# Optimization experiments

Measured on AMD Instinct MI355X. Metric: run time of the kernel, lower is better.

The kernel has to match this reference:

```python
import jax, jax.numpy as jnp
import numpy as np

LAYERS, BLOCKS = 10, 3
NL = LAYERS * BLOCKS
DC, RC, SC, CLASSES, K = 128, 128, 256, 256, 2
SR = 4096  # number of output samples sliced from the end
N, L, EN = 4, 8192, 16


def _conv1x1(x, w):
    # x: [N, Cin, L], w: [Cout, Cin] -> [N, Cout, L]
    return jnp.einsum('ncl,oc->nol', x, w)


def _condition(x, enc):
    # x: [N, C, L], enc: [N, C, En], L % En == 0; tiled periodic add (faithful to the view trick)
    n, c, l = x.shape
    en = enc.shape[2]
    return (x.reshape(n, c, l // en, en) + enc[:, :, None, :]).reshape(n, c, l)


def _dilated_causal_conv(x, w, d):
    # kernel_size=2 causal dilated conv. x: [N, Cin, L], w: [Cout, Cin, 2]
    xs = jnp.pad(x, ((0, 0), (0, 0), (d, 0)))[:, :, :x.shape[2]]  # x delayed by d
    return jnp.einsum('ncl,oc->nol', xs, w[:, :, 0]) + jnp.einsum('ncl,oc->nol', x, w[:, :, 1])


def setup_inputs() -> dict:
    key = jax.random.key(0)
    ks = jax.random.split(key, 12)
    s = 0.05
    return {
        'x': jax.random.normal(ks[0], (N, CLASSES, L), jnp.float32),
        'en': jax.random.normal(ks[1], (N, CLASSES, EN), jnp.float32),
        'start1_w': jax.random.normal(ks[2], (RC, CLASSES), jnp.float32) * s,
        'start2_w': jax.random.normal(ks[3], (SC, RC), jnp.float32) * s,
        'cond_w': jax.random.normal(ks[4], (NL, 2 * DC, CLASSES), jnp.float32) * s,
        'dil_w': jax.random.normal(ks[5], (NL, 2 * DC, RC, K), jnp.float32) * s,
        'res_w': jax.random.normal(ks[6], (NL, RC, DC), jnp.float32) * s,
        'skip_w': jax.random.normal(ks[7], (NL, SC, DC), jnp.float32) * s,
        'end1_w': jax.random.normal(ks[8], (CLASSES, SC), jnp.float32) * s,
        'end1_b': jnp.zeros((CLASSES,), jnp.float32),
        'end2_w': jax.random.normal(ks[9], (CLASSES, CLASSES), jnp.float32) * s,
        'end2_b': jnp.zeros((CLASSES,), jnp.float32),
    }


def reference(x, en, start1_w, start2_w, cond_w, dil_w, res_w, skip_w,
              end1_w, end1_b, end2_w, end2_b):
    l = _conv1x1(x, start1_w)          # [N, RC, L]
    s = _conv1x1(l, start2_w)          # [N, SC, L]
    for i in range(NL):
        dil = 2 ** (i % LAYERS)
        d = _dilated_causal_conv(l, dil_w[i], dil)      # [N, 2*DC, L]
        d = _condition(d, _conv1x1(en, cond_w[i]))
        g = jax.nn.sigmoid(d[:, :DC]) * jnp.tanh(d[:, DC:])  # gated, [N, DC, L]
        l = l + _conv1x1(g, res_w[i])
        s = s + _conv1x1(g, skip_w[i])
    s = jax.nn.relu(s)
    s = _conv1x1(s, end1_w) + end1_b[None, :, None]
    s = _condition(s, _conv1x1(en, end2_w) + end2_b[None, :, None])
    s = jax.nn.relu(s)
    return s[:, :, -SR:]
```

## Files before the change

kernel.cpp:

```cpp
#include <hip/hip_runtime.h>

typedef __bf16 bf16_t;
typedef __bf16 bf16x8 __attribute__((ext_vector_type(8)));
typedef __bf16 bf16x4 __attribute__((ext_vector_type(4)));
typedef float  f32x4  __attribute__((ext_vector_type(4)));
typedef int    i32x4  __attribute__((ext_vector_type(4)));

#define PL 136
#define PX 264

__device__ __forceinline__ f32x4 mfma16(bf16x8 a, bf16x8 b, f32x4 c) {
    return __builtin_amdgcn_mfma_f32_16x16x32_bf16(a, b, c, 0, 0, 0);
}

__device__ __forceinline__ void conv8(const float* __restrict__ src,
                                      bf16_t* __restrict__ dst,
                                      int g, int M, int K) {
    int MK8 = (M * K) >> 3;
    int lay = g / MK8;
    int r = g - lay * MK8;
    int lane = r & 63, rest = r >> 6;
    int KB = K >> 5;
    int kb = rest % KB, mt = rest / KB;
    int m = mt * 16 + (lane & 15);
    int k = kb * 32 + ((lane >> 4) << 3);
    const float* s = src + (size_t)lay * M * K + (size_t)m * K + k;
    f32x4 v0 = *(const f32x4*)s;
    f32x4 v1 = *(const f32x4*)(s + 4);
    bf16x8 o;
    o[0] = (bf16_t)v0[0]; o[1] = (bf16_t)v0[1]; o[2] = (bf16_t)v0[2]; o[3] = (bf16_t)v0[3];
    o[4] = (bf16_t)v1[0]; o[5] = (bf16_t)v1[1]; o[6] = (bf16_t)v1[2]; o[7] = (bf16_t)v1[3];
    *(bf16x8*)(dst + (size_t)g * 8) = o;
}

__global__ __launch_bounds__(256) void k_prep(
                       const float* __restrict__ rw, const float* __restrict__ kw,
                       const float* __restrict__ s1w, const float* __restrict__ s2w,
                       const float* __restrict__ e1w, const float* __restrict__ dwt,
                       const float* __restrict__ cond_w, const float* __restrict__ end2_w,
                       const float* __restrict__ end2_b, const float* __restrict__ en,
                       bf16_t* __restrict__ Ares, bf16_t* __restrict__ Askp,
                       bf16_t* __restrict__ A1, bf16_t* __restrict__ A2,
                       bf16_t* __restrict__ Ae, bf16_t* __restrict__ Adil,
                       float* __restrict__ cond_all, float* __restrict__ cond2) {
    if (blockIdx.x >= 1744) {
        __shared__ f32x4 en_s[1024];
        __shared__ f32x4 red[1024];
        int bi = blockIdx.x - 1744;
        int i = bi >> 4;
        int n = (bi >> 2) & 3;
        int og = bi & 3;
        int tid = threadIdx.x;
        const f32x4* ep = (const f32x4*)(en + (size_t)n * 4096);
        for (int idx = tid; idx < 1024; idx += 256) en_s[idx] = ep[idx];
        __syncthreads();
        int o_loc = tid >> 2, part = tid & 3;
        int o = og * 64 + o_loc;
        const float* W = (i < 30) ? cond_w + ((size_t)i * 256 + o) * 256
                                  : end2_w + (size_t)o * 256;
        const float* Wp = W + part * 64;
        f32x4 a0 = {0.f,0.f,0.f,0.f}, a1 = a0, a2 = a0, a3 = a0;
        for (int c = 0; c < 64; c += 4) {
            f32x4 wv = *(const f32x4*)(Wp + c);
            int cg = part * 64 + c;
            #pragma unroll
            for (int cc = 0; cc < 4; ++cc) {
                float wf = wv[cc];
                a0 += wf * en_s[(cg + cc) * 4 + 0];
                a1 += wf * en_s[(cg + cc) * 4 + 1];
                a2 += wf * en_s[(cg + cc) * 4 + 2];
                a3 += wf * en_s[(cg + cc) * 4 + 3];
            }
        }
        red[tid * 4 + 0] = a0; red[tid * 4 + 1] = a1;
        red[tid * 4 + 2] = a2; red[tid * 4 + 3] = a3;
        __syncthreads();
        if (tid < 64) {
            int o2 = og * 64 + tid;
            float bias = (i < 30) ? 0.f : end2_b[o2];
            float* dst = (i < 30) ? cond_all + (((size_t)i * 4 + n) * 256 + o2) * 16
                                  : cond2 + ((size_t)n * 256 + o2) * 16;
            f32x4* d4 = (f32x4*)dst;
            #pragma unroll
            for (int t = 0; t < 4; ++t) {
                f32x4 s = red[(tid * 4 + 0) * 4 + t] + red[(tid * 4 + 1) * 4 + t]
                        + red[(tid * 4 + 2) * 4 + t] + red[(tid * 4 + 3) * 4 + t];
                d4[t] = s + bias;
            }
        }
        return;
    }
    int g = blockIdx.x * 256 + threadIdx.x;
    if (g < 61440) { conv8(rw, Ares, g, 128, 128); return; }
    g -= 61440;
    if (g < 122880) { conv8(kw, Askp, g, 256, 128); return; }
    g -= 122880;
    if (g < 4096) { conv8(s1w, A1, g, 128, 256); return; }
    g -= 4096;
    if (g < 4096) { conv8(s2w, A2, g, 256, 128); return; }
    g -= 4096;
    if (g < 8192) { conv8(e1w, Ae, g, 256, 256); return; }
    g -= 8192;
    {
        int lay = g >> 13, r = g & 8191;
        int lane = r & 63, rest = r >> 6;
        int kb = rest & 7, mt = rest >> 3;
        int m = mt * 16 + (lane & 15);
        int k0 = kb * 32 + ((lane >> 4) << 3);
        int sel = (k0 < 128) ? 0 : 1;
        int kk = (k0 < 128) ? k0 : k0 - 128;
        const float* s = dwt + (((size_t)lay * 256 + m) * 128 + kk) * 2;
        f32x4 c0 = *(const f32x4*)(s);
        f32x4 c1 = *(const f32x4*)(s + 4);
        f32x4 c2 = *(const f32x4*)(s + 8);
        f32x4 c3 = *(const f32x4*)(s + 12);
        bf16x8 o;
        o[0] = (bf16_t)c0[sel];     o[1] = (bf16_t)c0[2 + sel];
        o[2] = (bf16_t)c1[sel];     o[3] = (bf16_t)c1[2 + sel];
        o[4] = (bf16_t)c2[sel];     o[5] = (bf16_t)c2[2 + sel];
        o[6] = (bf16_t)c3[sel];     o[7] = (bf16_t)c3[2 + sel];
        *(bf16x8*)(Adil + (size_t)lay * 65536 + (size_t)r * 8) = o;
    }
}

__global__ __launch_bounds__(512, 4) void k_start(
    const float* __restrict__ x, bf16_t* __restrict__ la, float* __restrict__ sbuf,
    const bf16_t* __restrict__ A1, const bf16_t* __restrict__ A2, int t_base)
{
    __shared__ __align__(16) bf16_t xt[64 * PX];
    __shared__ __align__(16) bf16_t l0[64 * PL];
    int tid = threadIdx.x;
    int n = blockIdx.y, t0 = t_base + blockIdx.x * 64;
    int lane = tid & 63, w = tid >> 6, i16 = lane & 15, q = lane >> 4;
    f32x4 z = {0.f,0.f,0.f,0.f};
    {
        int t = tid & 63;
        for (int c = tid >> 6; c < 256; c += 8)
            xt[t * PX + c] = (bf16_t)x[((size_t)n * 256 + c) * 8192 + t0 + t];
    }
    __syncthreads();
    f32x4 acc[4] = {z,z,z,z};
    #pragma unroll
    for (int kb = 0; kb < 8; ++kb) {
        int koff = kb * 32 + q * 8;
        bf16x8 bf[4];
        #pragma unroll
        for (int nt = 0; nt < 4; ++nt)
            bf[nt] = *(const bf16x8*)(xt + (nt * 16 + i16) * PX + koff);
        bf16x8 af = *(const bf16x8*)(A1 + (((size_t)w * 8 + kb) * 64 + lane) * 8);
        #pragma unroll
        for (int nt = 0; nt < 4; ++nt) acc[nt] = mfma16(af, bf[nt], acc[nt]);
    }
    #pragma unroll
    for (int nt = 0; nt < 4; ++nt)
        #pragma unroll
        for (int j = 0; j < 4; ++j)
            l0[(nt * 16 + i16) * PL + w * 16 + q * 4 + j] = (bf16_t)acc[nt][j];
    __syncthreads();
    {
        int r = tid >> 4, col = (tid & 15) * 8;
        #pragma unroll
        for (int p = 0; p < 2; ++p) {
            int rr = r + p * 32;
            *(i32x4*)(la + ((size_t)n * 8192 + t0 + rr) * 128 + col) =
                *(const i32x4*)(l0 + rr * PL + col);
        }
    }
    if (t0 >= 4096) {
        f32x4 a2[2][4] = {{z,z,z,z},{z,z,z,z}};
        #pragma unroll
        for (int kb = 0; kb < 4; ++kb) {
            int koff = kb * 32 + q * 8;
            bf16x8 bf[4];
            #pragma unroll
            for (int nt = 0; nt < 4; ++nt)
                bf[nt] = *(const bf16x8*)(l0 + (nt * 16 + i16) * PL + koff);
            #pragma unroll
            for (int mt2 = 0; mt2 < 2; ++mt2) {
                bf16x8 af = *(const bf16x8*)(A2 + ((((size_t)2 * w + mt2) * 4 + kb) * 64 + lane) * 8);
                #pragma unroll
                for (int nt = 0; nt < 4; ++nt) a2[mt2][nt] = mfma16(af, bf[nt], a2[mt2][nt]);
            }
        }
        float* sp = sbuf + (size_t)n * 256 * 4096 + (t0 - 4096);
        #pragma unroll
        for (int mt2 = 0; mt2 < 2; ++mt2)
            #pragma unroll
            for (int nt = 0; nt < 4; ++nt)
                #pragma unroll
                for (int j = 0; j < 4; ++j) {
                    int o = (2 * w + mt2) * 16 + q * 4 + j;
                    sp[(size_t)o * 4096 + nt * 16 + i16] = a2[mt2][nt][j];
                }
    }
}

template<int USEG>
__global__ __launch_bounds__(512, 4) void k_layer(
    const bf16_t* __restrict__ l_in, bf16_t* __restrict__ l_out,
    float* __restrict__ sbuf, bf16_t* __restrict__ Gl,
    const bf16_t* __restrict__ Ad, const bf16_t* __restrict__ Ar,
    const bf16_t* __restrict__ Ak, const float* __restrict__ condL,
    int dil, int t_base, int do_res)
{
    __shared__ __align__(16) bf16_t smA[64 * PL];
    __shared__ __align__(16) bf16_t sm2[32 * PL];
    int tid = threadIdx.x;
    int n = blockIdx.y, t0 = t_base + blockIdx.x * 32;
    int lane = tid & 63, w = tid >> 6, i16 = lane & 15, q = lane >> 4;
    f32x4 z = {0.f,0.f,0.f,0.f};
    const float* cond = condL + (size_t)n * 4096;
    int r = tid >> 4, col = (tid & 15) * 8;
    int c_base = w * 16 + q * 4;
    size_t base = (size_t)n * 8192;

    float cv_s[4], cv_t[4];
    #pragma unroll
    for (int j = 0; j < 4; ++j) {
        cv_s[j] = cond[(c_base + j) * 16 + i16];
        cv_t[j] = cond[(c_base + j + 128) * 16 + i16];
    }
    const bf16x8* AdF = (const bf16x8*)Ad;
    bf16x8 a_s[8], a_t[8];
    #pragma unroll
    for (int kb = 0; kb < 8; ++kb) {
        a_s[kb] = AdF[((size_t)w * 8 + kb) * 64 + lane];
        a_t[kb] = AdF[((size_t)(w + 8) * 8 + kb) * 64 + lane];
    }

    const bf16_t* curp;
    const bf16_t* delp;
    if (dil < 32) {
        int cnt = (32 + dil) * 16;
        for (int idx = tid; idx < cnt; idx += 512) {
            int rr = idx >> 4, c2 = (idx & 15) * 8;
            *(i32x4*)(smA + rr * PL + c2) =
                *(const i32x4*)(l_in + (base + t0 - dil + rr) * 128 + c2);
        }
        delp = smA; curp = smA + dil * PL;
    } else {
        *(i32x4*)(smA + r * PL + col) =
            *(const i32x4*)(l_in + (base + t0 + r) * 128 + col);
        int gp = t0 - dil + r;
        i32x4 v = {0, 0, 0, 0};
        if (gp >= 0) v = *(const i32x4*)(l_in + (base + gp) * 128 + col);
        *(i32x4*)(smA + (32 + r) * PL + col) = v;
        curp = smA; delp = smA + 32 * PL;
    }
    __syncthreads();

    f32x4 accs[2] = {z,z}, acct[2] = {z,z};
    #pragma unroll
    for (int kb = 0; kb < 8; ++kb) {
        const bf16_t* bsrc = (kb < 4) ? delp : curp;
        int koff = (kb & 3) * 32 + q * 8;
        bf16x8 bf[2];
        #pragma unroll
        for (int nt = 0; nt < 2; ++nt)
            bf[nt] = *(const bf16x8*)(bsrc + (nt * 16 + i16) * PL + koff);
        #pragma unroll
        for (int nt = 0; nt < 2; ++nt) {
            accs[nt] = mfma16(a_s[kb], bf[nt], accs[nt]);
            acct[nt] = mfma16(a_t[kb], bf[nt], acct[nt]);
        }
    }

    const bf16x8* ArF = (const bf16x8*)Ar;
    bf16x8 ar[4];
    if (do_res) {
        #pragma unroll
        for (int kb = 0; kb < 4; ++kb)
            ar[kb] = ArF[((size_t)w * 4 + kb) * 64 + lane];
    }

    {
        #pragma unroll
        for (int nt = 0; nt < 2; ++nt) {
            bf16x4 g4;
            #pragma unroll
            for (int j = 0; j < 4; ++j) {
                float vlo = accs[nt][j] + cv_s[j];
                float vhi = acct[nt][j] + cv_t[j];
                float sg = 1.0f / (1.0f + __expf(-vlo));
                float th = 1.0f - 2.0f / (1.0f + __expf(2.0f * vhi));
                g4[j] = (bf16_t)(sg * th);
            }
            *(bf16x4*)(sm2 + (nt * 16 + i16) * PL + c_base) = g4;
        }
    }
    __syncthreads();

    if (USEG) {
        if (t0 >= 4096) {
            int tt = ((tid & 256) >> 4) + (tid & 15);
            int cc = ((tid >> 6) & 3) * 32 + ((tid >> 4) & 3) * 8;
            bf16x8 gv = *(const bf16x8*)(sm2 + tt * PL + cc);
            *(bf16x8*)(Gl + ((size_t)n * 4096 + (t0 - 4096)) * 128 + tid * 8) = gv;
        }
    }

    f32x4 acc2[2] = {z,z};
    if (do_res || !USEG) {
        int do_skip = (!USEG) && (t0 >= 4096);
        f32x4 acc3[2][2] = {{z,z},{z,z}};
        const bf16x8* AkF = (const bf16x8*)Ak;
        #pragma unroll
        for (int kb = 0; kb < 4; ++kb) {
            int koff = kb * 32 + q * 8;
            bf16x8 bf[2];
            #pragma unroll
            for (int nt = 0; nt < 2; ++nt)
                bf[nt] = *(const bf16x8*)(sm2 + (nt * 16 + i16) * PL + koff);
            if (do_res) {
                #pragma unroll
                for (int nt = 0; nt < 2; ++nt) acc2[nt] = mfma16(ar[kb], bf[nt], acc2[nt]);
            }
            if (do_skip) {
                #pragma unroll
                for (int mt2 = 0; mt2 < 2; ++mt2) {
                    bf16x8 ak = AkF[((size_t)(2 * w + mt2) * 4 + kb) * 64 + lane];
                    #pragma unroll
                    for (int nt = 0; nt < 2; ++nt)
                        acc3[mt2][nt] = mfma16(ak, bf[nt], acc3[mt2][nt]);
                }
            }
        }
        if (do_skip) {
            float* sp = sbuf + (size_t)n * 256 * 4096 + (t0 - 4096);
            #pragma unroll
            for (int mt2 = 0; mt2 < 2; ++mt2)
                #pragma unroll
                for (int nt = 0; nt < 2; ++nt)
                    #pragma unroll
                    for (int j = 0; j < 4; ++j) {
                        int o = (2 * w + mt2) * 16 + q * 4 + j;
                        sp[(size_t)o * 4096 + nt * 16 + i16] += acc3[mt2][nt][j];
                    }
        }
    }

    if (do_res) {
        #pragma unroll
        for (int nt = 0; nt < 2; ++nt) {
            int trow = (nt * 16 + i16) * PL;
            bf16x4 lv = *(const bf16x4*)(curp + trow + c_base);
            bf16x4 o4;
            #pragma unroll
            for (int j = 0; j < 4; ++j)
                o4[j] = (bf16_t)((float)lv[j] + acc2[nt][j]);
            *(bf16x4*)(l_out + (base + t0 + nt * 16 + i16) * 128 + c_base) = o4;
        }
    }
}

#define SKIP_HALF(I, AKU, AKP, GW0, GW1)                                        \
    {                                                                           \
        const int i_ = (I);                                                     \
        if (i_ + 1 < 30) {                                                      \
            bf16_t* db = gbuf[(i_ + 1) & 1];                                    \
            *(i32x4*)(db + tid * 8) = GW0;                                      \
            *(i32x4*)(db + 4096 + tid * 8) = GW1;                               \
        }                                                                       \
        if (i_ + 3 < 30) {                                                      \
            const bf16_t* srcp = gb + (size_t)(i_ + 3) * GLS;                   \
            GW0 = *(const i32x4*)(srcp);                                        \
            GW1 = *(const i32x4*)(srcp + 4096);                                 \
        }                                                                       \
        if (i_ + 1 < 30) {                                                      \
            const bf16x8* An = (const bf16x8*)(Askp + (size_t)(i_ + 1) * 32768);\
            _Pragma("unroll")                                                   \
            for (int kb = 0; kb < 4; ++kb) {                                    \
                AKP[2 * kb]     = An[fi0 + kb * 64];                            \
                AKP[2 * kb + 1] = An[fi1 + kb * 64];                            \
            }                                                                   \
        }                                                                       \
        const bf16_t* gp_ = gbuf[i_ & 1];                                       \
        _Pragma("unroll")                                                       \
        for (int kb = 0; kb < 4; ++kb) {                                        \
            _Pragma("unroll")                                                   \
            for (int nt = 0; nt < 4; ++nt) {                                    \
                bf16x8 bfv = *(const bf16x8*)(gp_ + (nt >> 1) * 4096 +          \
                              (((nt & 1) * 4 + kb) * 64 + lane) * 8);           \
                acc[0][nt] = mfma16(AKU[2 * kb], bfv, acc[0][nt]);              \
                acc[1][nt] = mfma16(AKU[2 * kb + 1], bfv, acc[1][nt]);          \
            }                                                                   \
        }                                                                       \
        if (i_ + 1 < 30) {                                                      \
            asm volatile("s_waitcnt lgkmcnt(0)" ::: "memory");                  \
            __builtin_amdgcn_sched_barrier(0);                                  \
            __builtin_amdgcn_s_barrier();                                       \
            __builtin_amdgcn_sched_barrier(0);                                  \
        }                                                                       \
    }

__global__ __launch_bounds__(512, 2) void k_skip(
    const bf16_t* __restrict__ G, float* __restrict__ sbuf,
    const bf16_t* __restrict__ Askp)
{
    __shared__ __align__(16) bf16_t gbuf[2][8192];
    int tid = threadIdx.x;
    int n = blockIdx.y, t0 = blockIdx.x * 64;
    int lane = tid & 63, w = tid >> 6, i16 = lane & 15, q = lane >> 4;
    f32x4 z = {0.f,0.f,0.f,0.f};
    f32x4 acc[2][4] = {{z,z,z,z},{z,z,z,z}};
    const size_t GLS = (size_t)4 * 4096 * 128;
    const bf16_t* gb = G + ((size_t)n * 4096 + t0) * 128 + tid * 8;
    int fi0 = (2 * w) * 256 + lane;
    int fi1 = fi0 + 256;
    bf16x8 akA[8], akB[8];
    {
        const bf16x8* A0 = (const bf16x8*)Askp;
        #pragma unroll
        for (int kb = 0; kb < 4; ++kb) {
            akA[2 * kb]     = A0[fi0 + kb * 64];
            akA[2 * kb + 1] = A0[fi1 + kb * 64];
        }
    }
    i32x4 gA0, gA1, gB0, gB1;
    {
        i32x4 t0v = *(const i32x4*)(gb);
        i32x4 t1v = *(const i32x4*)(gb + 4096);
        *(i32x4*)(gbuf[0] + tid * 8) = t0v;
        *(i32x4*)(gbuf[0] + 4096 + tid * 8) = t1v;
    }
    gA0 = *(const i32x4*)(gb + 1 * GLS);
    gA1 = *(const i32x4*)(gb + 1 * GLS + 4096);
    gB0 = *(const i32x4*)(gb + 2 * GLS);
    gB1 = *(const i32x4*)(gb + 2 * GLS + 4096);
    __syncthreads();
    #pragma unroll 1
    for (int ii = 0; ii < 30; ii += 2) {
        SKIP_HALF(ii,     akA, akB, gA0, gA1)
        SKIP_HALF(ii + 1, akB, akA, gB0, gB1)
    }
    float* sp = sbuf + (size_t)n * 256 * 4096 + t0;
    #pragma unroll
    for (int mt2 = 0; mt2 < 2; ++mt2)
        #pragma unroll
        for (int nt = 0; nt < 4; ++nt)
            #pragma unroll
            for (int j = 0; j < 4; ++j) {
                int o = (2 * w + mt2) * 16 + q * 4 + j;
                sp[(size_t)o * 4096 + nt * 16 + i16] += acc[mt2][nt][j];
            }
}

__global__ __launch_bounds__(512) void k_end(
    const float* __restrict__ sbuf, float* __restrict__ out,
    const bf16_t* __restrict__ Ae, const float* __restrict__ cond2,
    const float* __restrict__ b1)
{
    __shared__ __align__(16) bf16_t st[64 * PX];
    __shared__ float c2[4096];
    __shared__ float b1s[256];
    int tid = threadIdx.x;
    int n = blockIdx.y, t0 = blockIdx.x * 64;
    int lane = tid & 63, w = tid >> 6, i16 = lane & 15, q = lane >> 4;
    f32x4 z = {0.f,0.f,0.f,0.f};
    {
        int t = tid & 63;
        for (int c = tid >> 6; c < 256; c += 8) {
            float v = sbuf[((size_t)n * 256 + c) * 4096 + t0 + t];
            st[t * PX + c] = (bf16_t)fmaxf(v, 0.f);
        }
        const f32x4* cc = (const f32x4*)(cond2 + (size_t)n * 4096);
        for (int idx = tid; idx < 1024; idx += 512) ((f32x4*)c2)[idx] = cc[idx];
        if (tid < 64) ((f32x4*)b1s)[tid] = ((const f32x4*)b1)[tid];
    }
    __syncthreads();
    f32x4 acc[2][4] = {{z,z,z,z},{z,z,z,z}};
    #pragma unroll
    for (int kb = 0; kb < 8; ++kb) {
        int koff = kb * 32 + q * 8;
        bf16x8 bf[4];
        #pragma unroll
        for (int nt = 0; nt < 4; ++nt)
            bf[nt] = *(const bf16x8*)(st + (nt * 16 + i16) * PX + koff);
        #pragma unroll
        for (int mt2 = 0; mt2 < 2; ++mt2) {
            bf16x8 af = *(const bf16x8*)(Ae + ((((size_t)2 * w + mt2) * 8 + kb) * 64 + lane) * 8);
            #pragma unroll
            for (int nt = 0; nt < 4; ++nt) acc[mt2][nt] = mfma16(af, bf[nt], acc[mt2][nt]);
        }
    }
    #pragma unroll
    for (int mt2 = 0; mt2 < 2; ++mt2)
        #pragma unroll
        for (int j = 0; j < 4; ++j) {
            int o = (2 * w + mt2) * 16 + q * 4 + j;
            float bb = b1s[o] + c2[o * 16 + i16];
            #pragma unroll
            for (int nt = 0; nt < 4; ++nt) {
                float v = acc[mt2][nt][j] + bb;
                out[((size_t)n * 256 + o) * 4096 + t0 + nt * 16 + i16] = fmaxf(v, 0.f);
            }
        }
}

extern "C" void kernel_launch(void* const* d_in, const int* in_sizes, int n_in,
                              void* d_out, int out_size, void* d_ws, size_t ws_size,
                              hipStream_t stream) {
    const float* x   = (const float*)d_in[0];
    const float* en  = (const float*)d_in[1];
    const float* s1w = (const float*)d_in[2];
    const float* s2w = (const float*)d_in[3];
    const float* cw  = (const float*)d_in[4];
    const float* dw  = (const float*)d_in[5];
    const float* rw  = (const float*)d_in[6];
    const float* kw  = (const float*)d_in[7];
    const float* e1w = (const float*)d_in[8];
    const float* e1b = (const float*)d_in[9];
    const float* e2w = (const float*)d_in[10];
    const float* e2b = (const float*)d_in[11];
    float* out = (float*)d_out;

    char* p = (char*)d_ws;
    auto take = [&](size_t bytes) {
        char* r = p;
        p += (bytes + 255) & ~(size_t)255;
        return r;
    };
    bf16_t* A1   = (bf16_t*)take((size_t)128 * 256 * 2);
    bf16_t* A2   = (bf16_t*)take((size_t)256 * 128 * 2);
    bf16_t* Ae   = (bf16_t*)take((size_t)256 * 256 * 2);
    bf16_t* Adil = (bf16_t*)take((size_t)30 * 65536 * 2);
    bf16_t* Ares = (bf16_t*)take((size_t)30 * 16384 * 2);
    bf16_t* Askp = (bf16_t*)take((size_t)30 * 32768 * 2);
    float*  condA= (float*)take((size_t)30 * 16384 * 4);
    float*  cond2= (float*)take((size_t)16384 * 4);
    bf16_t* la   = (bf16_t*)take((size_t)4 * 8192 * 128 * 2);
    bf16_t* lb   = (bf16_t*)take((size_t)4 * 8192 * 128 * 2);
    float*  sbuf = (float*)take((size_t)4 * 256 * 4096 * 4);
    bf16_t* G    = (bf16_t*)take((size_t)30 * 4 * 4096 * 128 * 2);
    bool useG = ((size_t)(p - (char*)d_ws) <= ws_size);

    k_prep<<<2240, 256, 0, stream>>>(rw, kw, s1w, s2w, e1w, dw,
                                     cw, e2w, e2b, en,
                                     Ares, Askp, A1, A2, Ae, Adil, condA, cond2);

    int a[30];
    a[29] = 4096;
    for (int i = 28; i >= 0; --i) {
        int nx = a[i + 1] - (1 << ((i + 1) % 10));
        a[i] = nx < 4096 ? (nx & ~63) : 4096;
    }

    k_start<<<dim3(127, 4), 512, 0, stream>>>(x, la, sbuf, A1, A2, 64);

    bf16_t* src = la;
    bf16_t* dst = lb;
    for (int i = 0; i < 30; ++i) {
        dim3 grid((8192 - a[i]) / 32, 4);
        if (useG)
            k_layer<1><<<grid, 512, 0, stream>>>(src, dst, sbuf,
                G + (size_t)i * 4 * 4096 * 128,
                Adil + (size_t)i * 65536, Ares + (size_t)i * 16384,
                Askp + (size_t)i * 32768, condA + (size_t)i * 16384,
                1 << (i % 10), a[i], i < 29 ? 1 : 0);
        else
            k_layer<0><<<grid, 512, 0, stream>>>(src, dst, sbuf, (bf16_t*)nullptr,
                Adil + (size_t)i * 65536, Ares + (size_t)i * 16384,
                Askp + (size_t)i * 32768, condA + (size_t)i * 16384,
                1 << (i % 10), a[i], i < 29 ? 1 : 0);
        bf16_t* t = src; src = dst; dst = t;
    }
    if (useG)
        k_skip<<<dim3(64, 4), 512, 0, stream>>>(G, sbuf, Askp);
    k_end<<<dim3(64, 4), 512, 0, stream>>>(sbuf, out, Ae, cond2, e1b);
}
```

Before: 626.6 us.

## Halve per-block time tile in layer kernel and use lighter barriers

```diff
diff --git a/kernel.cpp b/kernel.cpp
--- a/kernel.cpp
+++ b/kernel.cpp
@@ -11,6 +11,13 @@
 
 __device__ __forceinline__ f32x4 mfma16(bf16x8 a, bf16x8 b, f32x4 c) {
     return __builtin_amdgcn_mfma_f32_16x16x32_bf16(a, b, c, 0, 0, 0);
+}
+
+__device__ __forceinline__ void barrier_nodrain() {
+    asm volatile("s_waitcnt lgkmcnt(0)" ::: "memory");
+    __builtin_amdgcn_sched_barrier(0);
+    __builtin_amdgcn_s_barrier();
+    __builtin_amdgcn_sched_barrier(0);
 }
 
 __device__ __forceinline__ void conv8(const float* __restrict__ src,
@@ -62,14 +69,14 @@
         f32x4 a0 = {0.f,0.f,0.f,0.f}, a1 = a0, a2 = a0, a3 = a0;
         for (int c = 0; c < 64; c += 4) {
             f32x4 wv = *(const f32x4*)(Wp + c);
-            int cg = part * 64 + c;
+            int cg2 = part * 64 + c;
             #pragma unroll
             for (int cc = 0; cc < 4; ++cc) {
                 float wf = wv[cc];
-                a0 += wf * en_s[(cg + cc) * 4 + 0];
-                a1 += wf * en_s[(cg + cc) * 4 + 1];
-                a2 += wf * en_s[(cg + cc) * 4 + 2];
-                a3 += wf * en_s[(cg + cc) * 4 + 3];
+                a0 += wf * en_s[(cg2 + cc) * 4 + 0];
+                a1 += wf * en_s[(cg2 + cc) * 4 + 1];
+                a2 += wf * en_s[(cg2 + cc) * 4 + 2];
+                a3 += wf * en_s[(cg2 + cc) * 4 + 3];
             }
         }
         red[tid * 4 + 0] = a0; red[tid * 4 + 1] = a1;
@@ -203,14 +210,13 @@
     const bf16_t* __restrict__ Ak, const float* __restrict__ condL,
     int dil, int t_base, int do_res)
 {
-    __shared__ __align__(16) bf16_t smA[64 * PL];
-    __shared__ __align__(16) bf16_t sm2[32 * PL];
+    __shared__ __align__(16) bf16_t smA[32 * PL];
+    __shared__ __align__(16) bf16_t sm2[16 * PL];
     int tid = threadIdx.x;
-    int n = blockIdx.y, t0 = t_base + blockIdx.x * 32;
+    int n = blockIdx.y, t0 = t_base + blockIdx.x * 16;
     int lane = tid & 63, w = tid >> 6, i16 = lane & 15, q = lane >> 4;
     f32x4 z = {0.f,0.f,0.f,0.f};
     const float* cond = condL + (size_t)n * 4096;
-    int r = tid >> 4, col = (tid & 15) * 8;
     int c_base = w * 16 + q * 4;
     size_t base = (size_t)n * 8192;
 
@@ -230,8 +236,8 @@
 
     const bf16_t* curp;
     const bf16_t* delp;
-    if (dil < 32) {
-        int cnt = (32 + dil) * 16;
+    if (dil < 16) {
+        int cnt = (16 + dil) * 16;
         for (int idx = tid; idx < cnt; idx += 512) {
             int rr = idx >> 4, c2 = (idx & 15) * 8;
             *(i32x4*)(smA + rr * PL + c2) =
@@ -239,30 +245,28 @@
         }
         delp = smA; curp = smA + dil * PL;
     } else {
-        *(i32x4*)(smA + r * PL + col) =
-            *(const i32x4*)(l_in + (base + t0 + r) * 128 + col);
-        int gp = t0 - dil + r;
-        i32x4 v = {0, 0, 0, 0};
-        if (gp >= 0) v = *(const i32x4*)(l_in + (base + gp) * 128 + col);
-        *(i32x4*)(smA + (32 + r) * PL + col) = v;
-        curp = smA; delp = smA + 32 * PL;
-    }
-    __syncthreads();
-
-    f32x4 accs[2] = {z,z}, acct[2] = {z,z};
+        int r16 = (tid >> 4) & 15, c2 = (tid & 15) * 8;
+        if (tid < 256) {
+            *(i32x4*)(smA + r16 * PL + c2) =
+                *(const i32x4*)(l_in + (base + t0 + r16) * 128 + c2);
+        } else {
+            int gp = t0 - dil + r16;
+            i32x4 v = {0, 0, 0, 0};
+            if (gp >= 0) v = *(const i32x4*)(l_in + (base + gp) * 128 + c2);
+            *(i32x4*)(smA + (16 + r16) * PL + c2) = v;
+        }
+        curp = smA; delp = smA + 16 * PL;
+    }
+    barrier_nodrain();
+
+    f32x4 accs = z, acct = z;
     #pragma unroll
     for (int kb = 0; kb < 8; ++kb) {
         const bf16_t* bsrc = (kb < 4) ? delp : curp;
         int koff = (kb & 3) * 32 + q * 8;
-        bf16x8 bf[2];
-        #pragma unroll
-        for (int nt = 0; nt < 2; ++nt)
-            bf[nt] = *(const bf16x8*)(bsrc + (nt * 16 + i16) * PL + koff);
-        #pragma unroll
-        for (int nt = 0; nt < 2; ++nt) {
-            accs[nt] = mfma16(a_s[kb], bf[nt], accs[nt]);
-            acct[nt] = mfma16(a_t[kb], bf[nt], acct[nt]);
-        }
+        bf16x8 bf = *(const bf16x8*)(bsrc + i16 * PL + koff);
+        accs = mfma16(a_s[kb], bf, accs);
+        acct = mfma16(a_t[kb], bf, acct);
     }
 
     const bf16x8* ArF = (const bf16x8*)Ar;
@@ -274,54 +278,45 @@
     }
 
     {
-        #pragma unroll
-        for (int nt = 0; nt < 2; ++nt) {
-            bf16x4 g4;
-            #pragma unroll
-            for (int j = 0; j < 4; ++j) {
-                float vlo = accs[nt][j] + cv_s[j];
-                float vhi = acct[nt][j] + cv_t[j];
-                float sg = 1.0f / (1.0f + __expf(-vlo));
-                float th = 1.0f - 2.0f / (1.0f + __expf(2.0f * vhi));
-                g4[j] = (bf16_t)(sg * th);
-            }
-            *(bf16x4*)(sm2 + (nt * 16 + i16) * PL + c_base) = g4;
-        }
-    }
-    __syncthreads();
+        bf16x4 g4;
+        #pragma unroll
+        for (int j = 0; j < 4; ++j) {
+            float vlo = accs[j] + cv_s[j];
+            float vhi = acct[j] + cv_t[j];
+            float sg = 1.0f / (1.0f + __expf(-vlo));
+            float th = 1.0f - 2.0f / (1.0f + __expf(2.0f * vhi));
+            g4[j] = (bf16_t)(sg * th);
+        }
+        *(bf16x4*)(sm2 + i16 * PL + c_base) = g4;
+    }
+    barrier_nodrain();
 
     if (USEG) {
         if (t0 >= 4096) {
-            int tt = ((tid & 256) >> 4) + (tid & 15);
-            int cc = ((tid >> 6) & 3) * 32 + ((tid >> 4) & 3) * 8;
-            bf16x8 gv = *(const bf16x8*)(sm2 + tt * PL + cc);
-            *(bf16x8*)(Gl + ((size_t)n * 4096 + (t0 - 4096)) * 128 + tid * 8) = gv;
-        }
-    }
-
-    f32x4 acc2[2] = {z,z};
+            int rel = t0 - 4096;
+            bf16_t* gd = Gl + ((size_t)n * 4096 + (rel & ~31)) * 128
+                            + (size_t)((rel >> 4) & 1) * 2048 + tid * 4;
+            int lane6 = (tid >> 1) & 63;
+            int cc = (tid >> 7) * 32 + (lane6 >> 4) * 8 + (tid & 1) * 4;
+            *(bf16x4*)gd = *(const bf16x4*)(sm2 + (lane6 & 15) * PL + cc);
+        }
+    }
+
+    f32x4 acc2 = z;
     if (do_res || !USEG) {
         int do_skip = (!USEG) && (t0 >= 4096);
-        f32x4 acc3[2][2] = {{z,z},{z,z}};
+        f32x4 acc3[2] = {z, z};
         const bf16x8* AkF = (const bf16x8*)Ak;
         #pragma unroll
         for (int kb = 0; kb < 4; ++kb) {
             int koff = kb * 32 + q * 8;
-            bf16x8 bf[2];
-            #pragma unroll
-            for (int nt = 0; nt < 2; ++nt)
-                bf[nt] = *(const bf16x8*)(sm2 + (nt * 16 + i16) * PL + koff);
-            if (do_res) {
-                #pragma unroll
-                for (int nt = 0; nt < 2; ++nt) acc2[nt] = mfma16(ar[kb], bf[nt], acc2[nt]);
-            }
+            bf16x8 bf = *(const bf16x8*)(sm2 + i16 * PL + koff);
+            if (do_res) acc2 = mfma16(ar[kb], bf, acc2);
             if (do_skip) {
                 #pragma unroll
                 for (int mt2 = 0; mt2 < 2; ++mt2) {
                     bf16x8 ak = AkF[((size_t)(2 * w + mt2) * 4 + kb) * 64 + lane];
-                    #pragma unroll
-                    for (int nt = 0; nt < 2; ++nt)
-                        acc3[mt2][nt] = mfma16(ak, bf[nt], acc3[mt2][nt]);
+                    acc3[mt2] = mfma16(ak, bf, acc3[mt2]);
                 }
             }
         }
@@ -330,26 +325,20 @@
             #pragma unroll
             for (int mt2 = 0; mt2 < 2; ++mt2)
                 #pragma unroll
-                for (int nt = 0; nt < 2; ++nt)
-                    #pragma unroll
-                    for (int j = 0; j < 4; ++j) {
-                        int o = (2 * w + mt2) * 16 + q * 4 + j;
-                        sp[(size_t)o * 4096 + nt * 16 + i16] += acc3[mt2][nt][j];
-                    }
+                for (int j = 0; j < 4; ++j) {
+                    int o = (2 * w + mt2) * 16 + q * 4 + j;
+                    sp[(size_t)o * 4096 + i16] += acc3[mt2][j];
+                }
         }
     }
 
     if (do_res) {
-        #pragma unroll
-        for (int nt = 0; nt < 2; ++nt) {
-            int trow = (nt * 16 + i16) * PL;
-            bf16x4 lv = *(const bf16x4*)(curp + trow + c_base);
-            bf16x4 o4;
-            #pragma unroll
-            for (int j = 0; j < 4; ++j)
-                o4[j] = (bf16_t)((float)lv[j] + acc2[nt][j]);
-            *(bf16x4*)(l_out + (base + t0 + nt * 16 + i16) * 128 + c_base) = o4;
-        }
+        bf16x4 lv = *(const bf16x4*)(curp + i16 * PL + c_base);
+        bf16x4 o4;
+        #pragma unroll
+        for (int j = 0; j < 4; ++j)
+            o4[j] = (bf16_t)((float)lv[j] + acc2[j]);
+        *(bf16x4*)(l_out + (base + t0 + i16) * 128 + c_base) = o4;
     }
 }
 
@@ -550,7 +539,7 @@
     bf16_t* src = la;
     bf16_t* dst = lb;
     for (int i = 0; i < 30; ++i) {
-        dim3 grid((8192 - a[i]) / 32, 4);
+        dim3 grid((8192 - a[i]) / 16, 4);
         if (useG)
             k_layer<1><<<grid, 512, 0, stream>>>(src, dst, sbuf,
                 G + (size_t)i * 4 * 4096 * 128,
```

Result: slower. 689.0 us (+10.0%).
